# Kernel optimization log

Hardware: AMD Instinct MI355X
Metric: run time of the kernel (lower is better)

Reference implementation:

```python
import jax, jax.numpy as jnp
import numpy as np

EMB_DIM = 256
HEAD_DIM = 32


def setup_inputs() -> dict:
    key = jax.random.key(0)
    kx, kq, kk, kv = jax.random.split(key, 4)
    B, S = 4, 4096
    x = jax.random.normal(kx, (B, S, EMB_DIM), dtype=jnp.float32)
    # Linear(emb_dim, head_dim, bias=False): store as [emb_dim, head_dim]
    sc = 1.0 / np.sqrt(EMB_DIM)
    Wq = jax.random.normal(kq, (EMB_DIM, HEAD_DIM), dtype=jnp.float32) * sc
    Wk = jax.random.normal(kk, (EMB_DIM, HEAD_DIM), dtype=jnp.float32) * sc
    Wv = jax.random.normal(kv, (EMB_DIM, HEAD_DIM), dtype=jnp.float32) * sc
    return {"x": x, "Wq": Wq, "Wk": Wk, "Wv": Wv}


def reference(x, Wq, Wk, Wv):
    # single-head attention with POST-softmax scaling (as in source).
    # Dropout treated as identity (eval mode) for determinism.
    scaling = HEAD_DIM ** (-0.5)
    q = jnp.einsum('bse,ed->bsd', x, Wq)
    k = jnp.einsum('bse,ed->bsd', x, Wk)
    v = jnp.einsum('bse,ed->bsd', x, Wv)
    energy = jnp.einsum('bqd,bkd->bqk', q, k)  # [B,S,S]
    att = jax.nn.softmax(energy, axis=-1) * scaling
    out = jnp.einsum('bqk,bkd->bqd', att, v)
    return out
```

## Files before the change

kernel.cpp:

```cpp
#include <hip/hip_runtime.h>

#define EMB 256
#define HD 32
#define SEQ 4096
#define NSPLIT 16
#define KRANGE 256
#define NQROW 16384

typedef _Float16 half8 __attribute__((ext_vector_type(8)));
typedef _Float16 half4v __attribute__((ext_vector_type(4)));
typedef float floatx4 __attribute__((ext_vector_type(4)));
typedef float floatx16 __attribute__((ext_vector_type(16)));

#define L2E 1.44269504088896340736f
#define SCALING 0.17677669529663687f

__device__ __forceinline__ half8 mk8(unsigned a, unsigned b, unsigned c, unsigned d) {
  union { unsigned u[4]; half8 h; } z;
  z.u[0] = a; z.u[1] = b; z.u[2] = c; z.u[3] = d;
  return z.h;
}

__global__ __launch_bounds__(256) void prep_kernel(const float* __restrict__ Wq,
                                                   const float* __restrict__ Wk,
                                                   const float* __restrict__ Wv,
                                                   _Float16* __restrict__ wsw) {
  int gid = blockIdx.x * 256 + threadIdx.x;
  int j    = gid & 7;
  int lane = (gid >> 3) & 63;
  int kc   = (gid >> 9) & 7;
  int half = (gid >> 12) & 1;
  int mat  = gid >> 13;
  const float* W = (mat == 0) ? Wq : ((mat == 1) ? Wk : Wv);
  int n = lane & 15, quad = lane >> 4;
  int e = kc * 32 + quad * 8 + j;
  int d = n + half * 16;
  float v = W[e * HD + d];
  if (mat == 0) v *= L2E;
  wsw[gid] = (_Float16)v;
}

__global__ __launch_bounds__(256) void qkv_kernel(const float* __restrict__ x,
                                                  const _Float16* __restrict__ wsw,
                                                  _Float16* __restrict__ qw,
                                                  _Float16* __restrict__ kw,
                                                  _Float16* __restrict__ vt2) {
  int lane = threadIdx.x & 63, wave = threadIdx.x >> 6;
  int n = lane & 15, quad = lane >> 4;
  int mat = blockIdx.y;
  int rowbase = blockIdx.x * 64 + wave * 16;

  floatx4 c0 = {0,0,0,0}, c1 = {0,0,0,0};

#pragma unroll
  for (int kc = 0; kc < 8; ++kc) {
    const float* xp = x + (rowbase + n) * EMB + kc * 32 + quad * 8;
    float4 xa = *(const float4*)(xp);
    float4 xb = *(const float4*)(xp + 4);
    half8 a;
    a[0] = (_Float16)xa.x; a[1] = (_Float16)xa.y; a[2] = (_Float16)xa.z; a[3] = (_Float16)xa.w;
    a[4] = (_Float16)xb.x; a[5] = (_Float16)xb.y; a[6] = (_Float16)xb.z; a[7] = (_Float16)xb.w;
    half8 b0 = *(const half8*)(wsw + (((mat * 2 + 0) * 8 + kc) << 9) + (lane << 3));
    half8 b1 = *(const half8*)(wsw + (((mat * 2 + 1) * 8 + kc) << 9) + (lane << 3));
    c0 = __builtin_amdgcn_mfma_f32_16x16x32_f16(a, b0, c0, 0, 0, 0);
    c1 = __builtin_amdgcn_mfma_f32_16x16x32_f16(a, b1, c1, 0, 0, 0);
  }

  if (mat == 2) {
    int b = rowbase >> 12;
    int s0 = rowbase & (SEQ - 1);
    _Float16* vb = vt2 + (size_t)b * SEQ * HD;
#pragma unroll
    for (int r = 0; r < 4; ++r) {
      int s = s0 + quad * 4 + r;
      int blk = (s >> 3) << 8, sl = s & 7;
      vb[blk + n * 8 + sl]        = (_Float16)c0[r];
      vb[blk + (n + 16) * 8 + sl] = (_Float16)c1[r];
    }
  } else {
    _Float16* dst = (mat == 0) ? qw : kw;
#pragma unroll
    for (int r = 0; r < 4; ++r) {
      int row = rowbase + quad * 4 + r;
      dst[row * HD + n]      = (_Float16)c0[r];
      dst[row * HD + n + 16] = (_Float16)c1[r];
    }
  }
}

__global__ __launch_bounds__(256, 4) void attn_kernel(const _Float16* __restrict__ q,
                                                      const _Float16* __restrict__ k,
                                                      const _Float16* __restrict__ vt2,
                                                      _Float16* __restrict__ Op,
                                                      float* __restrict__ Mp,
                                                      float* __restrict__ Lp) {
  const int t = threadIdx.x;
  const int w = t >> 6, lane = t & 63;
  const int n2 = lane & 31, h = lane >> 5;
  const int qb = blockIdx.x & 127;
  const int sp = blockIdx.x >> 7;
  const int b = qb >> 5;
  const int qrow0 = qb * 128 + w * 32;
  const int key0 = sp * KRANGE;

  const _Float16* kb = k   + (size_t)(b * SEQ + key0) * HD;
  const _Float16* vb = vt2 + (size_t)b * SEQ * HD + (size_t)key0 * HD;

  half8 qb0 = *(const half8*)(q + (qrow0 + n2) * HD + h * 8);
  half8 qb1 = *(const half8*)(q + (qrow0 + n2) * HD + 16 + h * 8);

  floatx16 o;
#pragma unroll
  for (int r = 0; r < 16; ++r) o[r] = 0.f;
  const floatx16 zero16 = o;
  float m = -__builtin_huge_valf();
  float l = 0.f;

  half8 ka0 = *(const half8*)(kb + (size_t)n2 * HD + h * 8);
  half8 ka1 = *(const half8*)(kb + (size_t)n2 * HD + 16 + h * 8);
  half8 va0 = *(const half8*)(vb + h * 256 + n2 * 8);
  half8 va1 = *(const half8*)(vb + 512 + h * 256 + n2 * 8);

#pragma unroll
  for (int kt = 0; kt < KRANGE / 32; ++kt) {
    half8 nka0, nka1, nva0, nva1;
    if (kt + 1 < KRANGE / 32) {
      const _Float16* kn = kb + (size_t)((kt + 1) * 32 + n2) * HD;
      const _Float16* vn = vb + (kt + 1) * 1024;
      nka0 = *(const half8*)(kn + h * 8);
      nka1 = *(const half8*)(kn + 16 + h * 8);
      nva0 = *(const half8*)(vn + h * 256 + n2 * 8);
      nva1 = *(const half8*)(vn + 512 + h * 256 + n2 * 8);
    }

    floatx16 s = __builtin_amdgcn_mfma_f32_32x32x16_f16(ka0, qb0, zero16, 0, 0, 0);
    s = __builtin_amdgcn_mfma_f32_32x32x16_f16(ka1, qb1, s, 0, 0, 0);

    floatx4 s0 = {s[0], s[1], s[2], s[3]};
    floatx4 s1 = {s[4], s[5], s[6], s[7]};
    floatx4 s2 = {s[8], s[9], s[10], s[11]};
    floatx4 s3 = {s[12], s[13], s[14], s[15]};
    floatx4 t01 = __builtin_elementwise_max(s0, s1);
    floatx4 t23 = __builtin_elementwise_max(s2, s3);
    floatx4 t4  = __builtin_elementwise_max(t01, t23);
    float mm = fmaxf(fmaxf(t4[0], t4[1]), fmaxf(t4[2], t4[3]));
    mm = fmaxf(mm, __shfl_xor(mm, 32));
    float mnew = fmaxf(m, mm);
    float alpha = __builtin_amdgcn_exp2f(m - mnew);
    m = mnew;

    float p[16];
#pragma unroll
    for (int r = 0; r < 16; ++r) p[r] = __builtin_amdgcn_exp2f(s[r] - mnew);
    unsigned pk[8];
#pragma unroll
    for (int g = 0; g < 8; ++g)
      pk[g] = __builtin_bit_cast(unsigned, __builtin_amdgcn_cvt_pkrtz(p[2 * g], p[2 * g + 1]));

    float ps = ((p[0] + p[1]) + (p[2] + p[3])) + ((p[4] + p[5]) + (p[6] + p[7]))
             + ((p[8] + p[9]) + (p[10] + p[11])) + ((p[12] + p[13]) + (p[14] + p[15]));
    ps += __shfl_xor(ps, 32);
    l = l * alpha + ps;

#pragma unroll
    for (int r = 0; r < 16; ++r) o[r] *= alpha;

    unsigned tmp0 = h ? pk[0] : pk[2];
    unsigned tmp1 = h ? pk[1] : pk[3];
    unsigned tmp2 = h ? pk[4] : pk[6];
    unsigned tmp3 = h ? pk[5] : pk[7];
    unsigned ex0 = (unsigned)__shfl_xor((int)tmp0, 32);
    unsigned ex1 = (unsigned)__shfl_xor((int)tmp1, 32);
    unsigned ex2 = (unsigned)__shfl_xor((int)tmp2, 32);
    unsigned ex3 = (unsigned)__shfl_xor((int)tmp3, 32);
    half8 B0 = h ? mk8(ex0, ex1, pk[2], pk[3]) : mk8(pk[0], pk[1], ex0, ex1);
    half8 B1 = h ? mk8(ex2, ex3, pk[6], pk[7]) : mk8(pk[4], pk[5], ex2, ex3);

    o = __builtin_amdgcn_mfma_f32_32x32x16_f16(va0, B0, o, 0, 0, 0);
    o = __builtin_amdgcn_mfma_f32_32x32x16_f16(va1, B1, o, 0, 0, 0);

    ka0 = nka0; ka1 = nka1; va0 = nva0; va1 = nva1;
  }

  size_t obase = ((size_t)(sp * NQROW + qrow0) + n2) * 32;
#pragma unroll
  for (int bb = 0; bb < 4; ++bb) {
    half4v pv;
    pv[0] = (_Float16)o[4 * bb + 0];
    pv[1] = (_Float16)o[4 * bb + 1];
    pv[2] = (_Float16)o[4 * bb + 2];
    pv[3] = (_Float16)o[4 * bb + 3];
    *(half4v*)&Op[obase + 8 * bb + 4 * h] = pv;
  }
  if (h == 0) {
    int mi = sp * NQROW + qrow0 + n2;
    Mp[mi] = m;
    Lp[mi] = l;
  }
}

__global__ __launch_bounds__(256) void combine_kernel(const _Float16* __restrict__ Op,
                                                      const float* __restrict__ Mp,
                                                      const float* __restrict__ Lp,
                                                      float* __restrict__ out) {
  int gid = blockIdx.x * 256 + threadIdx.x;
  int dc = gid & 7, qrow = gid >> 3;
  float mv[NSPLIT];
  float ms = -__builtin_huge_valf();
#pragma unroll
  for (int sp = 0; sp < NSPLIT; ++sp) {
    mv[sp] = Mp[sp * NQROW + qrow];
    ms = fmaxf(ms, mv[sp]);
  }
  float L = 0.f;
  floatx4 O = {0.f, 0.f, 0.f, 0.f};
#pragma unroll
  for (int sp = 0; sp < NSPLIT; ++sp) {
    float ww = __builtin_amdgcn_exp2f(mv[sp] - ms);
    L += ww * Lp[sp * NQROW + qrow];
    half4v ov = *(const half4v*)&Op[((size_t)(sp * NQROW + qrow)) * 32 + dc * 4];
#pragma unroll
    for (int r = 0; r < 4; ++r) O[r] += ww * (float)ov[r];
  }
  float inv = SCALING / L;
  floatx4 res = {O[0] * inv, O[1] * inv, O[2] * inv, O[3] * inv};
  *(floatx4*)&out[qrow * HD + dc * 4] = res;
}

extern "C" void kernel_launch(void* const* d_in, const int* in_sizes, int n_in,
                              void* d_out, int out_size, void* d_ws, size_t ws_size,
                              hipStream_t stream) {
  const float* x  = (const float*)d_in[0];
  const float* Wq = (const float*)d_in[1];
  const float* Wk = (const float*)d_in[2];
  const float* Wv = (const float*)d_in[3];
  float* out = (float*)d_out;

  _Float16* wsw = (_Float16*)d_ws;
  _Float16* qw  = wsw + 24576;
  _Float16* kw  = qw + NQROW * HD;
  _Float16* vt2 = kw + NQROW * HD;
  _Float16* Op  = vt2 + NQROW * HD;
  float* Mp = (float*)(Op + (size_t)NSPLIT * NQROW * 32);
  float* Lp = Mp + NSPLIT * NQROW;

  prep_kernel<<<96, 256, 0, stream>>>(Wq, Wk, Wv, wsw);
  qkv_kernel<<<dim3(256, 3), 256, 0, stream>>>(x, wsw, qw, kw, vt2);
  attn_kernel<<<2048, 256, 0, stream>>>(qw, kw, vt2, Op, Mp, Lp);
  combine_kernel<<<512, 256, 0, stream>>>(Op, Mp, Lp, out);
}
```

Before: 99.98 us.

## Defer softmax rescaling, fuse QKV projection, halve split count, use permlane swaps

The attention loop now rescales the running max only when a new row max exceeds the current one by a threshold (lazy rescaling). It uses permlane32 swaps for the P-operand exchange and fdot2 to sum the packed fp16 probabilities. Key splits drop from 16 to 8, so each block covers 512 keys and the combine pass has fewer partials to merge. The QKV projection is fused into one launch that computes all three matrices and reuses each x load. Risks include fp16 overflow from deferred rescaling, since p can reach 2^8, and lower occupancy with fewer blocks.

```diff
diff --git a/kernel.cpp b/kernel.cpp
--- a/kernel.cpp
+++ b/kernel.cpp
@@ -3,22 +3,56 @@
 #define EMB 256
 #define HD 32
 #define SEQ 4096
-#define NSPLIT 16
-#define KRANGE 256
+#define NSPLIT 8
+#define KRANGE 512
+#define NT (KRANGE / 32)
 #define NQROW 16384
 
 typedef _Float16 half8 __attribute__((ext_vector_type(8)));
 typedef _Float16 half4v __attribute__((ext_vector_type(4)));
+typedef _Float16 half2v __attribute__((ext_vector_type(2)));
 typedef float floatx4 __attribute__((ext_vector_type(4)));
 typedef float floatx16 __attribute__((ext_vector_type(16)));
+typedef unsigned uint2v __attribute__((ext_vector_type(2)));
 
 #define L2E 1.44269504088896340736f
 #define SCALING 0.17677669529663687f
+#define DEFER_THR 8.0f
 
 __device__ __forceinline__ half8 mk8(unsigned a, unsigned b, unsigned c, unsigned d) {
   union { unsigned u[4]; half8 h; } z;
   z.u[0] = a; z.u[1] = b; z.u[2] = c; z.u[3] = d;
   return z.h;
+}
+
+__device__ __forceinline__ void plswap(unsigned& a, unsigned& b) {
+#if __has_builtin(__builtin_amdgcn_permlane32_swap)
+  uint2v r = __builtin_amdgcn_permlane32_swap(a, b, false, false);
+  a = r[0]; b = r[1];
+#else
+  unsigned sa = (unsigned)__shfl_xor((int)a, 32);
+  unsigned sb = (unsigned)__shfl_xor((int)b, 32);
+  bool hi = (threadIdx.x & 32) != 0;
+  unsigned na = hi ? sb : a;
+  unsigned nb = hi ? b : sa;
+  a = na; b = nb;
+#endif
+}
+__device__ __forceinline__ float plswap_red_max(float x) {
+  return fmaxf(x, __shfl_xor(x, 32));
+}
+__device__ __forceinline__ float plswap_red_add(float x) {
+  return x + __shfl_xor(x, 32);
+}
+
+__device__ __forceinline__ float sum2(unsigned pk, float acc) {
+  half2v a = __builtin_bit_cast(half2v, pk);
+#if __has_builtin(__builtin_amdgcn_fdot2)
+  half2v one; one[0] = (_Float16)1.f; one[1] = (_Float16)1.f;
+  return __builtin_amdgcn_fdot2(a, one, acc, false);
+#else
+  return acc + (float)a[0] + (float)a[1];
+#endif
 }
 
 __global__ __launch_bounds__(256) void prep_kernel(const float* __restrict__ Wq,
@@ -47,10 +81,11 @@
                                                   _Float16* __restrict__ vt2) {
   int lane = threadIdx.x & 63, wave = threadIdx.x >> 6;
   int n = lane & 15, quad = lane >> 4;
-  int mat = blockIdx.y;
   int rowbase = blockIdx.x * 64 + wave * 16;
 
-  floatx4 c0 = {0,0,0,0}, c1 = {0,0,0,0};
+  floatx4 cq0 = {0,0,0,0}, cq1 = {0,0,0,0};
+  floatx4 ck0 = {0,0,0,0}, ck1 = {0,0,0,0};
+  floatx4 cv0 = {0,0,0,0}, cv1 = {0,0,0,0};
 
 #pragma unroll
   for (int kc = 0; kc < 8; ++kc) {
@@ -60,31 +95,35 @@
     half8 a;
     a[0] = (_Float16)xa.x; a[1] = (_Float16)xa.y; a[2] = (_Float16)xa.z; a[3] = (_Float16)xa.w;
     a[4] = (_Float16)xb.x; a[5] = (_Float16)xb.y; a[6] = (_Float16)xb.z; a[7] = (_Float16)xb.w;
-    half8 b0 = *(const half8*)(wsw + (((mat * 2 + 0) * 8 + kc) << 9) + (lane << 3));
-    half8 b1 = *(const half8*)(wsw + (((mat * 2 + 1) * 8 + kc) << 9) + (lane << 3));
-    c0 = __builtin_amdgcn_mfma_f32_16x16x32_f16(a, b0, c0, 0, 0, 0);
-    c1 = __builtin_amdgcn_mfma_f32_16x16x32_f16(a, b1, c1, 0, 0, 0);
-  }
-
-  if (mat == 2) {
-    int b = rowbase >> 12;
-    int s0 = rowbase & (SEQ - 1);
-    _Float16* vb = vt2 + (size_t)b * SEQ * HD;
-#pragma unroll
-    for (int r = 0; r < 4; ++r) {
-      int s = s0 + quad * 4 + r;
-      int blk = (s >> 3) << 8, sl = s & 7;
-      vb[blk + n * 8 + sl]        = (_Float16)c0[r];
-      vb[blk + (n + 16) * 8 + sl] = (_Float16)c1[r];
-    }
-  } else {
-    _Float16* dst = (mat == 0) ? qw : kw;
-#pragma unroll
-    for (int r = 0; r < 4; ++r) {
-      int row = rowbase + quad * 4 + r;
-      dst[row * HD + n]      = (_Float16)c0[r];
-      dst[row * HD + n + 16] = (_Float16)c1[r];
-    }
+    const _Float16* wp = wsw + (kc << 9) + (lane << 3);
+    half8 bq0 = *(const half8*)(wp);
+    half8 bq1 = *(const half8*)(wp + (8  << 9));
+    half8 bk0 = *(const half8*)(wp + (16 << 9));
+    half8 bk1 = *(const half8*)(wp + (24 << 9));
+    half8 bv0 = *(const half8*)(wp + (32 << 9));
+    half8 bv1 = *(const half8*)(wp + (40 << 9));
+    cq0 = __builtin_amdgcn_mfma_f32_16x16x32_f16(a, bq0, cq0, 0, 0, 0);
+    cq1 = __builtin_amdgcn_mfma_f32_16x16x32_f16(a, bq1, cq1, 0, 0, 0);
+    ck0 = __builtin_amdgcn_mfma_f32_16x16x32_f16(a, bk0, ck0, 0, 0, 0);
+    ck1 = __builtin_amdgcn_mfma_f32_16x16x32_f16(a, bk1, ck1, 0, 0, 0);
+    cv0 = __builtin_amdgcn_mfma_f32_16x16x32_f16(a, bv0, cv0, 0, 0, 0);
+    cv1 = __builtin_amdgcn_mfma_f32_16x16x32_f16(a, bv1, cv1, 0, 0, 0);
+  }
+
+  int b = rowbase >> 12;
+  int s0 = rowbase & (SEQ - 1);
+  _Float16* vbase = vt2 + (size_t)b * SEQ * HD;
+#pragma unroll
+  for (int r = 0; r < 4; ++r) {
+    int row = rowbase + quad * 4 + r;
+    qw[row * HD + n]      = (_Float16)cq0[r];
+    qw[row * HD + n + 16] = (_Float16)cq1[r];
+    kw[row * HD + n]      = (_Float16)ck0[r];
+    kw[row * HD + n + 16] = (_Float16)ck1[r];
+    int s = s0 + quad * 4 + r;
+    int blk = (s >> 3) << 8, sl = s & 7;
+    vbase[blk + n * 8 + sl]        = (_Float16)cv0[r];
+    vbase[blk + (n + 16) * 8 + sl] = (_Float16)cv1[r];
   }
 }
 
@@ -106,14 +145,15 @@
   const _Float16* kb = k   + (size_t)(b * SEQ + key0) * HD;
   const _Float16* vb = vt2 + (size_t)b * SEQ * HD + (size_t)key0 * HD;
 
-  half8 qb0 = *(const half8*)(q + (qrow0 + n2) * HD + h * 8);
-  half8 qb1 = *(const half8*)(q + (qrow0 + n2) * HD + 16 + h * 8);
+  half8 qf0 = *(const half8*)(q + (qrow0 + n2) * HD + h * 8);
+  half8 qf1 = *(const half8*)(q + (qrow0 + n2) * HD + 16 + h * 8);
 
   floatx16 o;
 #pragma unroll
   for (int r = 0; r < 16; ++r) o[r] = 0.f;
   const floatx16 zero16 = o;
   float m = -__builtin_huge_valf();
+  float mtrue = -__builtin_huge_valf();
   float l = 0.f;
 
   half8 ka0 = *(const half8*)(kb + (size_t)n2 * HD + h * 8);
@@ -121,20 +161,18 @@
   half8 va0 = *(const half8*)(vb + h * 256 + n2 * 8);
   half8 va1 = *(const half8*)(vb + 512 + h * 256 + n2 * 8);
 
-#pragma unroll
-  for (int kt = 0; kt < KRANGE / 32; ++kt) {
-    half8 nka0, nka1, nva0, nva1;
-    if (kt + 1 < KRANGE / 32) {
-      const _Float16* kn = kb + (size_t)((kt + 1) * 32 + n2) * HD;
-      const _Float16* vn = vb + (kt + 1) * 1024;
-      nka0 = *(const half8*)(kn + h * 8);
-      nka1 = *(const half8*)(kn + 16 + h * 8);
-      nva0 = *(const half8*)(vn + h * 256 + n2 * 8);
-      nva1 = *(const half8*)(vn + 512 + h * 256 + n2 * 8);
-    }
-
-    floatx16 s = __builtin_amdgcn_mfma_f32_32x32x16_f16(ka0, qb0, zero16, 0, 0, 0);
-    s = __builtin_amdgcn_mfma_f32_32x32x16_f16(ka1, qb1, s, 0, 0, 0);
+#pragma unroll 4
+  for (int kt = 0; kt < NT; ++kt) {
+    int nxt = (kt + 1) & (NT - 1);
+    const _Float16* kn = kb + (size_t)(nxt * 32 + n2) * HD;
+    const _Float16* vn = vb + nxt * 1024;
+    half8 nka0 = *(const half8*)(kn + h * 8);
+    half8 nka1 = *(const half8*)(kn + 16 + h * 8);
+    half8 nva0 = *(const half8*)(vn + h * 256 + n2 * 8);
+    half8 nva1 = *(const half8*)(vn + 512 + h * 256 + n2 * 8);
+
+    floatx16 s = __builtin_amdgcn_mfma_f32_32x32x16_f16(ka0, qf0, zero16, 0, 0, 0);
+    s = __builtin_amdgcn_mfma_f32_32x32x16_f16(ka1, qf1, s, 0, 0, 0);
 
     floatx4 s0 = {s[0], s[1], s[2], s[3]};
     floatx4 s1 = {s[4], s[5], s[6], s[7]};
@@ -144,57 +182,58 @@
     floatx4 t23 = __builtin_elementwise_max(s2, s3);
     floatx4 t4  = __builtin_elementwise_max(t01, t23);
     float mm = fmaxf(fmaxf(t4[0], t4[1]), fmaxf(t4[2], t4[3]));
-    mm = fmaxf(mm, __shfl_xor(mm, 32));
-    float mnew = fmaxf(m, mm);
-    float alpha = __builtin_amdgcn_exp2f(m - mnew);
-    m = mnew;
-
-    float p[16];
-#pragma unroll
-    for (int r = 0; r < 16; ++r) p[r] = __builtin_amdgcn_exp2f(s[r] - mnew);
+    mm = plswap_red_max(mm);
+    mtrue = fmaxf(mtrue, mm);
+
+    if (__any(mm > m + DEFER_THR)) {
+      float mnew = fmaxf(m, mm);
+      float alpha = __builtin_amdgcn_exp2f(m - mnew);
+      m = mnew;
+#pragma unroll
+      for (int r = 0; r < 16; ++r) o[r] *= alpha;
+      l *= alpha;
+    }
+
     unsigned pk[8];
 #pragma unroll
-    for (int g = 0; g < 8; ++g)
-      pk[g] = __builtin_bit_cast(unsigned, __builtin_amdgcn_cvt_pkrtz(p[2 * g], p[2 * g + 1]));
-
-    float ps = ((p[0] + p[1]) + (p[2] + p[3])) + ((p[4] + p[5]) + (p[6] + p[7]))
-             + ((p[8] + p[9]) + (p[10] + p[11])) + ((p[12] + p[13]) + (p[14] + p[15]));
-    ps += __shfl_xor(ps, 32);
-    l = l * alpha + ps;
-
-#pragma unroll
-    for (int r = 0; r < 16; ++r) o[r] *= alpha;
-
-    unsigned tmp0 = h ? pk[0] : pk[2];
-    unsigned tmp1 = h ? pk[1] : pk[3];
-    unsigned tmp2 = h ? pk[4] : pk[6];
-    unsigned tmp3 = h ? pk[5] : pk[7];
-    unsigned ex0 = (unsigned)__shfl_xor((int)tmp0, 32);
-    unsigned ex1 = (unsigned)__shfl_xor((int)tmp1, 32);
-    unsigned ex2 = (unsigned)__shfl_xor((int)tmp2, 32);
-    unsigned ex3 = (unsigned)__shfl_xor((int)tmp3, 32);
-    half8 B0 = h ? mk8(ex0, ex1, pk[2], pk[3]) : mk8(pk[0], pk[1], ex0, ex1);
-    half8 B1 = h ? mk8(ex2, ex3, pk[6], pk[7]) : mk8(pk[4], pk[5], ex2, ex3);
-
-    o = __builtin_amdgcn_mfma_f32_32x32x16_f16(va0, B0, o, 0, 0, 0);
-    o = __builtin_amdgcn_mfma_f32_32x32x16_f16(va1, B1, o, 0, 0, 0);
+    for (int g = 0; g < 8; ++g) {
+      float p0 = __builtin_amdgcn_exp2f(s[2 * g] - m);
+      float p1 = __builtin_amdgcn_exp2f(s[2 * g + 1] - m);
+      pk[g] = __builtin_bit_cast(unsigned, __builtin_amdgcn_cvt_pkrtz(p0, p1));
+    }
+
+    float lA = sum2(pk[3], sum2(pk[2], sum2(pk[1], sum2(pk[0], 0.f))));
+    float lB = sum2(pk[7], sum2(pk[6], sum2(pk[5], sum2(pk[4], 0.f))));
+    l += lA + lB;
+
+    unsigned b00 = pk[0], b02 = pk[2]; plswap(b00, b02);
+    unsigned b01 = pk[1], b03 = pk[3]; plswap(b01, b03);
+    unsigned b10 = pk[4], b12 = pk[6]; plswap(b10, b12);
+    unsigned b11 = pk[5], b13 = pk[7]; plswap(b11, b13);
+
+    o = __builtin_amdgcn_mfma_f32_32x32x16_f16(va0, mk8(b00, b01, b02, b03), o, 0, 0, 0);
+    o = __builtin_amdgcn_mfma_f32_32x32x16_f16(va1, mk8(b10, b11, b12, b13), o, 0, 0, 0);
 
     ka0 = nka0; ka1 = nka1; va0 = nva0; va1 = nva1;
   }
+
+  float scale = __builtin_amdgcn_exp2f(m - mtrue);
+  l *= scale;
+  l = plswap_red_add(l);
 
   size_t obase = ((size_t)(sp * NQROW + qrow0) + n2) * 32;
 #pragma unroll
   for (int bb = 0; bb < 4; ++bb) {
     half4v pv;
-    pv[0] = (_Float16)o[4 * bb + 0];
-    pv[1] = (_Float16)o[4 * bb + 1];
-    pv[2] = (_Float16)o[4 * bb + 2];
-    pv[3] = (_Float16)o[4 * bb + 3];
+    pv[0] = (_Float16)(o[4 * bb + 0] * scale);
+    pv[1] = (_Float16)(o[4 * bb + 1] * scale);
+    pv[2] = (_Float16)(o[4 * bb + 2] * scale);
+    pv[3] = (_Float16)(o[4 * bb + 3] * scale);
     *(half4v*)&Op[obase + 8 * bb + 4 * h] = pv;
   }
   if (h == 0) {
     int mi = sp * NQROW + qrow0 + n2;
-    Mp[mi] = m;
+    Mp[mi] = mtrue;
     Lp[mi] = l;
   }
 }
@@ -245,7 +284,7 @@
   float* Lp = Mp + NSPLIT * NQROW;
 
   prep_kernel<<<96, 256, 0, stream>>>(Wq, Wk, Wv, wsw);
-  qkv_kernel<<<dim3(256, 3), 256, 0, stream>>>(x, wsw, qw, kw, vt2);
-  attn_kernel<<<2048, 256, 0, stream>>>(qw, kw, vt2, Op, Mp, Lp);
+  qkv_kernel<<<256, 256, 0, stream>>>(x, wsw, qw, kw, vt2);
+  attn_kernel<<<1024, 256, 0, stream>>>(qw, kw, vt2, Op, Mp, Lp);
   combine_kernel<<<512, 256, 0, stream>>>(Op, Mp, Lp, out);
 }
```

Result: no change. 98.13 us (-1.9%).
